# Optimization experiments

Hardware: AMD Instinct MI355X
Metric: run time of the kernel (lower is better)

## Reference

```python
import jax, jax.numpy as jnp
import numpy as np

N, E, NF, EF = 2048, 65536, 128, 64
HID, NH, HD, FF, L = 256, 8, 32, 1024, 4
OUT, MAXN = 1280, 4096


def setup_inputs() -> dict:
    key = jax.random.key(0)
    ks = iter(jax.random.split(key, 64))
    def rn(shape, s=0.02):
        return jax.random.normal(next(ks), shape, jnp.float32) * s
    inp = dict(
        node_features=jax.random.normal(next(ks), (N, NF), jnp.float32),
        edge_features=jax.random.normal(next(ks), (E, EF), jnp.float32),
        edge_index=jax.random.randint(next(ks), (2, E), 0, N),
        W_node=rn((NF, HID)), b_node=jnp.zeros((HID,)),
        W_edge=rn((EF, HID)), b_edge=jnp.zeros((HID,)),
        pos_emb=rn((MAXN, HID), 1.0),
        Wq=rn((L, HID, HID)), bq=jnp.zeros((L, HID)),
        Wk=rn((L, HID, HID)), bk=jnp.zeros((L, HID)),
        Wv=rn((L, HID, HID)), bv=jnp.zeros((L, HID)),
        Wo=rn((L, HID, HID)), bo=jnp.zeros((L, HID)),
        Wep=rn((L, HID, NH)), bep=jnp.zeros((L, NH)),
        Wf1=rn((L, HID, FF)), bf1=jnp.zeros((L, FF)),
        Wf2=rn((L, FF, HID)), bf2=jnp.zeros((L, HID)),
        g1=jnp.ones((L, HID)), be1=jnp.zeros((L, HID)),
        g2=jnp.ones((L, HID)), be2=jnp.zeros((L, HID)),
        g_ln=jnp.ones((HID,)), b_ln=jnp.zeros((HID,)),
        Wp1=rn((HID, HID)), bp1=jnp.zeros((HID,)),
        Wp2=rn((HID, 1)), bp2=jnp.zeros((1,)),
        Wo1=rn((3 * HID, 2 * HID)), bo1=jnp.zeros((2 * HID,)),
        Wo2=rn((2 * HID, OUT)), bo2=jnp.zeros((OUT,)),
    )
    return inp


def _ln(x, g, b, eps=1e-5):
    m = x.mean(-1, keepdims=True)
    v = ((x - m) ** 2).mean(-1, keepdims=True)
    return (x - m) * jax.lax.rsqrt(v + eps) * g + b


def reference(node_features, edge_features, edge_index, W_node, b_node, W_edge,
              b_edge, pos_emb, Wq, bq, Wk, bk, Wv, bv, Wo, bo, Wep, bep,
              Wf1, bf1, Wf2, bf2, g1, be1, g2, be2, g_ln, b_ln,
              Wp1, bp1, Wp2, bp2, Wo1, bo1, Wo2, bo2):
    n = node_features.shape[0]
    src, dst = edge_index[0], edge_index[1]
    scale = float(np.sqrt(HD))
    # node encoding + learned positional embedding (n <= max_nodes path)
    x = node_features @ W_node + b_node + pos_emb[:n]
    edge_attr = edge_features @ W_edge + b_edge  # [E, HID]
    # symmetric adjacency mask with self-loops
    adj = jnp.zeros((n, n), bool).at[src, dst].set(True).at[dst, src].set(True)
    adj = adj.at[jnp.arange(n), jnp.arange(n)].set(True)
    for i in range(L):
        Q = (x @ Wq[i] + bq[i]).reshape(n, NH, HD)
        K = (x @ Wk[i] + bk[i]).reshape(n, NH, HD)
        V = (x @ Wv[i] + bv[i]).reshape(n, NH, HD)
        scores = jnp.einsum('nhd,mhd->nmh', Q, K) / scale  # [n, n, NH]
        ebias = edge_attr @ Wep[i] + bep[i]  # [E, NH]
        scores = scores.at[src, dst].add(ebias)  # accumulating scatter, same as per-edge loop
        scores = jnp.where(adj[:, None, :], scores.transpose(0, 2, 1), -jnp.inf)  # [n, NH, n]
        attn = jax.nn.softmax(scores, axis=-1)
        ctx = jnp.einsum('nhm,mhd->nhd', attn, V).reshape(n, HID)
        a = ctx @ Wo[i] + bo[i]
        x = _ln(x + a, g1[i], be1[i])
        f = jax.nn.gelu(x @ Wf1[i] + bf1[i], approximate=False) @ Wf2[i] + bf2[i]
        x = _ln(x + f, g2[i], be2[i])
    x = _ln(x, g_ln, b_ln)
    # global pooling (batch=None path): mean / max / attention
    mean_p = x.mean(0, keepdims=True)
    max_p = x.max(0, keepdims=True)
    aw = jax.nn.softmax(jnp.tanh(x @ Wp1 + bp1) @ Wp2 + bp2, axis=0)  # [n, 1]
    attn_p = (x * aw).sum(0, keepdims=True)
    g = jnp.concatenate([mean_p, max_p, attn_p], axis=1)  # [1, 3*HID]
    out = jax.nn.relu(g @ Wo1 + bo1) @ Wo2 + bo2  # [1, OUT]
    return out
```

## Files before the change

kernel.cpp:

```cpp
#include <hip/hip_runtime.h>
#include <math.h>

#define NNODE 2048
#define NEDGE 65536
#define HIDN  256
#define NHEAD 8
#define HDIM  32
#define FFD   1024
#define NLAYER 4
#define OUTD  1280
#define NNZ_MAX (2*NEDGE + NNODE)

typedef __attribute__((ext_vector_type(8))) short bf16x8;
typedef __attribute__((ext_vector_type(4))) float f32x4;

__device__ __forceinline__ unsigned short f2b(float f) {
    unsigned u = __float_as_uint(f);
    unsigned r = (u + 0x7fffu + ((u >> 16) & 1u)) >> 16;
    return (unsigned short)r;
}
__device__ __forceinline__ float b2f(unsigned short u) {
    return __uint_as_float((unsigned)u << 16);
}

template<int K, int EPI, int OUT>
__global__ __launch_bounds__(256)
void mgemm(const unsigned short* __restrict__ A, const unsigned short* __restrict__ Bt,
           const float* __restrict__ bias, const float* __restrict__ extra,
           float* __restrict__ Cf, unsigned short* __restrict__ Cb,
           int M, int N, const float* __restrict__ Wp2, float* __restrict__ sred)
{
    __shared__ __align__(16) unsigned short As[64 * 40];
    __shared__ __align__(16) unsigned short Bs[64 * 40];
    int tid = threadIdx.x;
    int bm0 = blockIdx.y * 64, bn0 = blockIdx.x * 64;
    int wave = tid >> 6, lane = tid & 63;
    int wm = (wave >> 1) * 32, wn = (wave & 1) * 32;
    int srow = tid >> 2, skoff = (tid & 3) * 8;
    int lrow = lane & 15, quad = lane >> 4;
    const unsigned short* ap = A  + (size_t)(bm0 + srow) * K + skoff;
    const unsigned short* bp = Bt + (size_t)(bn0 + srow) * K + skoff;
    uint4 av = *(const uint4*)ap;
    uint4 bv = *(const uint4*)bp;
    f32x4 acc[2][2] = {};
    constexpr int NC = K / 32;
    #pragma unroll 8
    for (int c = 0; c < NC; ++c) {
        *(uint4*)(&As[srow*40 + skoff]) = av;
        *(uint4*)(&Bs[srow*40 + skoff]) = bv;
        __syncthreads();
        if (c + 1 < NC) {
            av = *(const uint4*)(ap + (c+1)*32);
            bv = *(const uint4*)(bp + (c+1)*32);
        }
        bf16x8 af[2], bfr[2];
        #pragma unroll
        for (int i = 0; i < 2; i++) af[i]  = *(const bf16x8*)(&As[(wm + i*16 + lrow)*40 + quad*8]);
        #pragma unroll
        for (int j = 0; j < 2; j++) bfr[j] = *(const bf16x8*)(&Bs[(wn + j*16 + lrow)*40 + quad*8]);
        #pragma unroll
        for (int i = 0; i < 2; i++)
            #pragma unroll
            for (int j = 0; j < 2; j++)
                acc[i][j] = __builtin_amdgcn_mfma_f32_16x16x32_bf16(af[i], bfr[j], acc[i][j], 0, 0, 0);
        __syncthreads();
    }
    if (EPI == 4) {
        #pragma unroll
        for (int i = 0; i < 2; i++) {
            #pragma unroll
            for (int r = 0; r < 4; r++) {
                int row = bm0 + wm + i*16 + quad*4 + r;
                float ps = 0.f;
                #pragma unroll
                for (int j = 0; j < 2; j++) {
                    int col = bn0 + wn + j*16 + lrow;
                    float v = tanhf(acc[i][j][r] + bias[col]);
                    ps += v * Wp2[col];
                }
                ps += __shfl_xor(ps, 1);
                ps += __shfl_xor(ps, 2);
                ps += __shfl_xor(ps, 4);
                ps += __shfl_xor(ps, 8);
                if (lrow == 0) atomicAdd(&sred[row], ps);
            }
        }
        return;
    }
    #pragma unroll
    for (int i = 0; i < 2; i++)
        #pragma unroll
        for (int j = 0; j < 2; j++) {
            int col = bn0 + wn + j*16 + lrow;
            float bvv = bias[col];
            #pragma unroll
            for (int r = 0; r < 4; r++) {
                int row = bm0 + wm + i*16 + quad*4 + r;
                float v = acc[i][j][r] + bvv;
                if (EPI == 1) v = 0.5f * v * (1.f + erff(v * 0.70710678118654752f));
                else if (EPI == 2) v = tanhf(v);
                else if (EPI == 3) v += extra[(size_t)row*N + col];
                if (OUT == 0 || OUT == 2) Cf[(size_t)row*N + col] = v;
                if (OUT == 1 || OUT == 2) Cb[(size_t)row*N + col] = f2b(v);
            }
        }
}

__global__ __launch_bounds__(256)
void transpose_all(const float* __restrict__ Wq, const float* __restrict__ Wk,
                   const float* __restrict__ Wv, const float* __restrict__ Wo,
                   const float* __restrict__ Wf1, const float* __restrict__ Wf2,
                   const float* __restrict__ W_node, const float* __restrict__ Wp1,
                   unsigned short* __restrict__ WqkvT, unsigned short* __restrict__ WoT,
                   unsigned short* __restrict__ Wf1T, unsigned short* __restrict__ Wf2T,
                   unsigned short* __restrict__ WnT, unsigned short* __restrict__ Wp1T)
{
    __shared__ unsigned short tile[32][33];
    int bid = blockIdx.x;
    const float* s; unsigned short* d; int K, N, n0, k0;
    if (bid < 1024) {
        int mat = bid >> 6, rem = bid & 63;
        int m4 = mat & 3, l = mat >> 2;
        s = (m4 == 0 ? Wq : m4 == 1 ? Wk : m4 == 2 ? Wv : Wo) + (size_t)l * 65536;
        d = (m4 < 3) ? WqkvT + (size_t)l*196608 + (size_t)m4*65536
                     : WoT + (size_t)l*65536;
        K = 256; N = 256; n0 = (rem & 7) * 32; k0 = (rem >> 3) * 32;
    } else if (bid < 2048) {
        int idx = bid - 1024; int l = idx >> 8, rem = idx & 255;
        s = Wf1 + (size_t)l*262144; d = Wf1T + (size_t)l*262144;
        K = 256; N = 1024; n0 = (rem & 31) * 32; k0 = (rem >> 5) * 32;
    } else if (bid < 3072) {
        int idx = bid - 2048; int l = idx >> 8, rem = idx & 255;
        s = Wf2 + (size_t)l*262144; d = Wf2T + (size_t)l*262144;
        K = 1024; N = 256; n0 = (rem & 7) * 32; k0 = (rem >> 3) * 32;
    } else if (bid < 3104) {
        int rem = bid - 3072;
        s = W_node; d = WnT;
        K = 128; N = 256; n0 = (rem & 7) * 32; k0 = (rem >> 3) * 32;
    } else {
        int rem = bid - 3104;
        s = Wp1; d = Wp1T;
        K = 256; N = 256; n0 = (rem & 7) * 32; k0 = (rem >> 3) * 32;
    }
    int tx = threadIdx.x & 31, ty = threadIdx.x >> 5;
    #pragma unroll
    for (int i = 0; i < 4; i++)
        tile[ty + i*8][tx] = f2b(s[(size_t)(k0 + ty + i*8) * N + n0 + tx]);
    __syncthreads();
    #pragma unroll
    for (int i = 0; i < 4; i++)
        d[(size_t)(n0 + ty + i*8) * K + k0 + tx] = tile[tx][ty + i*8];
}

__global__ void misc_prep(const float* __restrict__ nf, unsigned short* __restrict__ nf_b,
                          const float* __restrict__ bq, const float* __restrict__ bk,
                          const float* __restrict__ bv, float* __restrict__ bqkv)
{
    int t = blockIdx.x * 256 + threadIdx.x;
    if (t < NNODE*128) {
        nf_b[t] = f2b(nf[t]);
    } else {
        int u = t - NNODE*128;
        if (u < NLAYER*768) {
            int l = u / 768, j = u % 768;
            float v = (j < 256) ? bq[l*256 + j] : (j < 512 ? bk[l*256 + j - 256] : bv[l*256 + j - 512]);
            bqkv[u] = v;
        }
    }
}

__global__ void adj_build(const int* __restrict__ src, const int* __restrict__ dst,
                          unsigned* __restrict__ adjbits)
{
    int t = blockIdx.x * blockDim.x + threadIdx.x;
    if (t < NEDGE) {
        int s = src[t], d = dst[t];
        atomicOr(&adjbits[(size_t)s*64 + (d >> 5)], 1u << (d & 31));
        atomicOr(&adjbits[(size_t)d*64 + (s >> 5)], 1u << (s & 31));
    }
    if (t < NNODE)
        atomicOr(&adjbits[(size_t)t*64 + (t >> 5)], 1u << (t & 31));
}

__global__ void row_rank(const unsigned* __restrict__ adjbits,
                         unsigned* __restrict__ rowcum, int* __restrict__ deg)
{
    int i = blockIdx.x * blockDim.x + threadIdx.x;
    if (i >= NNODE) return;
    unsigned c = 0;
    for (int w = 0; w < 64; w++) {
        rowcum[i*64 + w] = c;
        c += __popc(adjbits[i*64 + w]);
    }
    deg[i] = (int)c;
}

__global__ __launch_bounds__(256)
void scan_kernel(const int* __restrict__ deg, int* __restrict__ rowoff)
{
    __shared__ int part[256];
    int tid = threadIdx.x;
    int base = tid * 8;
    int local[8]; int s = 0;
    #pragma unroll
    for (int k = 0; k < 8; k++) { local[k] = s; s += deg[base + k]; }
    part[tid] = s;
    __syncthreads();
    for (int off = 1; off < 256; off <<= 1) {
        int v = (tid >= off) ? part[tid - off] : 0;
        __syncthreads();
        part[tid] += v;
        __syncthreads();
    }
    int pre = (tid == 0) ? 0 : part[tid - 1];
    #pragma unroll
    for (int k = 0; k < 8; k++) rowoff[base + k] = pre + local[k];
    if (tid == 255) rowoff[NNODE] = part[255];
}

__global__ __launch_bounds__(256)
void fill_cols(const unsigned* __restrict__ adjbits, const int* __restrict__ rowoff,
               const unsigned* __restrict__ rowcum, int* __restrict__ cols)
{
    int t = blockIdx.x * 256 + threadIdx.x;
    int i = t >> 6, w = t & 63;
    unsigned bits = adjbits[(size_t)i*64 + w];
    int base = rowoff[i] + (int)rowcum[(size_t)i*64 + w];
    while (bits) {
        int b = __ffs(bits) - 1;
        cols[base++] = w*32 + b;
        bits &= bits - 1;
    }
}

__global__ void wcomb_kernel(const float* __restrict__ W_edge, const float* __restrict__ b_edge,
                             const float* __restrict__ Wep, const float* __restrict__ bep,
                             float* __restrict__ Wcomb, float* __restrict__ bcomb)
{
    int t = blockIdx.x * blockDim.x + threadIdx.x;
    if (t < 64*32) {
        int k = t >> 5, lh = t & 31, l = lh >> 3, h = lh & 7;
        float acc = 0.f;
        for (int c = 0; c < HIDN; c++)
            acc += W_edge[k*HIDN + c] * Wep[l*HIDN*NHEAD + c*NHEAD + h];
        Wcomb[k*32 + lh] = acc;
    } else if (t < 64*32 + 32) {
        int lh = t - 64*32, l = lh >> 3, h = lh & 7;
        float acc = bep[l*NHEAD + h];
        for (int c = 0; c < HIDN; c++)
            acc += b_edge[c] * Wep[l*HIDN*NHEAD + c*NHEAD + h];
        bcomb[lh] = acc;
    }
}

__global__ __launch_bounds__(256)
void edge_bias_scatter(const float* __restrict__ ef, const float* __restrict__ Wcomb,
                       const float* __restrict__ bcomb,
                       const int* __restrict__ src, const int* __restrict__ dst,
                       const unsigned* __restrict__ adjbits,
                       const unsigned* __restrict__ rowcum,
                       const int* __restrict__ rowoff, float* __restrict__ bias_csr)
{
    __shared__ float Wl[64*32];
    __shared__ float bl[32];
    int tid = threadIdx.x;
    for (int k = tid; k < 64*32; k += 256) Wl[k] = Wcomb[k];
    if (tid < 32) bl[tid] = bcomb[tid];
    __syncthreads();
    int t = blockIdx.x * 256 + tid;
    int e = t >> 5, lh = t & 31;
    const float* f = ef + (size_t)e * 64;
    float acc = bl[lh];
    #pragma unroll
    for (int k = 0; k < 64; k++) acc += f[k] * Wl[k*32 + lh];
    int s = src[e], d = dst[e];
    unsigned wbits = adjbits[(size_t)s*64 + (d >> 5)];
    int rank = (int)rowcum[(size_t)s*64 + (d >> 5)] + __popc(wbits & ((1u << (d & 31)) - 1u));
    int slot = rowoff[s] + rank;
    atomicAdd(&bias_csr[(size_t)slot*32 + lh], acc);
}

__global__ __launch_bounds__(256)
void attn_kernel(const unsigned short* __restrict__ QKVb, const int* __restrict__ rowoff,
                 const int* __restrict__ cols, const float* __restrict__ bias_csr,
                 unsigned short* __restrict__ ctxb, int layer)
{
    __shared__ float mS[4][8], lS[4][8];
    __shared__ __align__(16) float accS[4][256];
    int i = blockIdx.x;
    int tid = threadIdx.x;
    int w = tid >> 6, lane = tid & 63;
    int h = lane >> 3;
    int off = lane * 4;
    ushort4 qu = *(const ushort4*)(QKVb + (size_t)i*768 + off);
    float4 qf = { b2f(qu.x), b2f(qu.y), b2f(qu.z), b2f(qu.w) };
    int start = rowoff[i], end = rowoff[i+1];
    int lh0 = layer * 8 + h;
    float m = -INFINITY, l = 0.f;
    float4 acc = {0.f, 0.f, 0.f, 0.f};
    for (int c0 = start + w; c0 < end; c0 += 256) {
        int myslot = c0 + 4*lane;
        int mycol = (myslot < end) ? cols[myslot] : 0;
        int lim = min(end, c0 + 256);
        int it = 0;
        for (int slot = c0; slot < lim; slot += 4, ++it) {
            int j = __shfl(mycol, it);
            ushort4 ku = *(const ushort4*)(QKVb + (size_t)j*768 + 256 + off);
            float s = qf.x*b2f(ku.x) + qf.y*b2f(ku.y) + qf.z*b2f(ku.z) + qf.w*b2f(ku.w);
            s += __shfl_xor(s, 1);
            s += __shfl_xor(s, 2);
            s += __shfl_xor(s, 4);
            s = s * 0.17677669529663687f + bias_csr[(size_t)slot*32 + lh0];
            float mn = fmaxf(m, s);
            float sc = __expf(m - mn);
            float p  = __expf(s - mn);
            ushort4 vu = *(const ushort4*)(QKVb + (size_t)j*768 + 512 + off);
            acc.x = acc.x*sc + p*b2f(vu.x);
            acc.y = acc.y*sc + p*b2f(vu.y);
            acc.z = acc.z*sc + p*b2f(vu.z);
            acc.w = acc.w*sc + p*b2f(vu.w);
            l = l*sc + p;
            m = mn;
        }
    }
    if ((lane & 7) == 0) { mS[w][h] = m; lS[w][h] = l; }
    *(float4*)&accS[w][off] = acc;
    __syncthreads();
    if (w == 0) {
        float m0 = mS[0][h], m1 = mS[1][h], m2 = mS[2][h], m3 = mS[3][h];
        float mx = fmaxf(fmaxf(m0, m1), fmaxf(m2, m3));
        float e0 = (m0 == -INFINITY) ? 0.f : __expf(m0 - mx);
        float e1 = (m1 == -INFINITY) ? 0.f : __expf(m1 - mx);
        float e2 = (m2 == -INFINITY) ? 0.f : __expf(m2 - mx);
        float e3 = (m3 == -INFINITY) ? 0.f : __expf(m3 - mx);
        float ls = lS[0][h]*e0 + lS[1][h]*e1 + lS[2][h]*e2 + lS[3][h]*e3;
        float4 a0 = *(float4*)&accS[0][off];
        float4 a1 = *(float4*)&accS[1][off];
        float4 a2 = *(float4*)&accS[2][off];
        float4 a3 = *(float4*)&accS[3][off];
        float inv = 1.f / ls;
        ushort4 o;
        o.x = f2b((a0.x*e0 + a1.x*e1 + a2.x*e2 + a3.x*e3) * inv);
        o.y = f2b((a0.y*e0 + a1.y*e1 + a2.y*e2 + a3.y*e3) * inv);
        o.z = f2b((a0.z*e0 + a1.z*e1 + a2.z*e2 + a3.z*e3) * inv);
        o.w = f2b((a0.w*e0 + a1.w*e1 + a2.w*e2 + a3.w*e3) * inv);
        *(ushort4*)(ctxb + (size_t)i*HIDN + off) = o;
    }
}

template<bool RES>
__global__ __launch_bounds__(256)
void ln_kernel(float* __restrict__ x, const float* __restrict__ r,
               const float* __restrict__ g, const float* __restrict__ b,
               unsigned short* __restrict__ xb)
{
    __shared__ float lds[4];
    int row = blockIdx.x, c = threadIdx.x;
    float v = x[(size_t)row*HIDN + c];
    if (RES) v += r[(size_t)row*HIDN + c];
    float s = v;
    for (int mm = 1; mm < 64; mm <<= 1) s += __shfl_xor(s, mm);
    if ((c & 63) == 0) lds[c >> 6] = s;
    __syncthreads();
    float mean = (lds[0] + lds[1] + lds[2] + lds[3]) * (1.f / HIDN);
    __syncthreads();
    float dv = v - mean;
    float qq = dv * dv;
    for (int mm = 1; mm < 64; mm <<= 1) qq += __shfl_xor(qq, mm);
    if ((c & 63) == 0) lds[c >> 6] = qq;
    __syncthreads();
    float var = (lds[0] + lds[1] + lds[2] + lds[3]) * (1.f / HIDN);
    float rs = rsqrtf(var + 1e-5f);
    float o = dv * rs * g[c] + b[c];
    x[(size_t)row*HIDN + c] = o;
    xb[(size_t)row*HIDN + c] = f2b(o);
}

__global__ __launch_bounds__(256)
void pool_fused(const float* __restrict__ x, const float* __restrict__ sred,
                float* __restrict__ g)
{
    __shared__ float sl[NNODE];
    __shared__ float red[4];
    __shared__ float l1[4], l2[4], l3[4];
    int c = blockIdx.x, tid = threadIdx.x;
    float mxs = -INFINITY;
    for (int r = tid; r < NNODE; r += 256) {
        float v = sred[r];
        sl[r] = v;
        mxs = fmaxf(mxs, v);
    }
    for (int mm = 1; mm < 64; mm <<= 1) mxs = fmaxf(mxs, __shfl_xor(mxs, mm));
    if ((tid & 63) == 0) red[tid >> 6] = mxs;
    __syncthreads();
    mxs = fmaxf(fmaxf(red[0], red[1]), fmaxf(red[2], red[3]));
    __syncthreads();
    float ss = 0.f;
    for (int r = tid; r < NNODE; r += 256) ss += __expf(sl[r] - mxs);
    for (int mm = 1; mm < 64; mm <<= 1) ss += __shfl_xor(ss, mm);
    if ((tid & 63) == 0) red[tid >> 6] = ss;
    __syncthreads();
    ss = red[0] + red[1] + red[2] + red[3];
    float inv = 1.f / ss;
    float sm = 0.f, mx = -INFINITY, ap = 0.f;
    for (int r = tid; r < NNODE; r += 256) {
        float v = x[(size_t)r*HIDN + c];
        sm += v;
        mx = fmaxf(mx, v);
        ap += v * __expf(sl[r] - mxs) * inv;
    }
    for (int mm = 1; mm < 64; mm <<= 1) {
        sm += __shfl_xor(sm, mm);
        mx = fmaxf(mx, __shfl_xor(mx, mm));
        ap += __shfl_xor(ap, mm);
    }
    if ((tid & 63) == 0) { int w = tid >> 6; l1[w] = sm; l2[w] = mx; l3[w] = ap; }
    __syncthreads();
    if (tid == 0) {
        sm = l1[0] + l1[1] + l1[2] + l1[3];
        mx = fmaxf(fmaxf(l2[0], l2[1]), fmaxf(l2[2], l2[3]));
        ap = l3[0] + l3[1] + l3[2] + l3[3];
        g[c]          = sm * (1.f / NNODE);
        g[HIDN + c]   = mx;
        g[2*HIDN + c] = ap;
    }
}

__global__ __launch_bounds__(512)
void head_fused(const float* __restrict__ g, const float* __restrict__ Wo1,
                const float* __restrict__ bo1, const float* __restrict__ Wo2,
                const float* __restrict__ bo2, float* __restrict__ out)
{
    __shared__ float gs[3*HIDN];
    __shared__ float hs[512];
    int tid = threadIdx.x;
    for (int k = tid; k < 3*HIDN; k += 512) gs[k] = g[k];
    __syncthreads();
    float acc = bo1[tid];
    for (int k = 0; k < 3*HIDN; k++) acc += gs[k] * Wo1[(size_t)k*512 + tid];
    hs[tid] = fmaxf(acc, 0.f);
    __syncthreads();
    for (int j = tid; j < OUTD; j += 512) {
        float a2 = bo2[j];
        for (int k = 0; k < 512; k++) a2 += hs[k] * Wo2[(size_t)k*OUTD + j];
        out[j] = a2;
    }
}

extern "C" void kernel_launch(void* const* d_in, const int* in_sizes, int n_in,
                              void* d_out, int out_size, void* d_ws, size_t ws_size,
                              hipStream_t stream)
{
    const float* node_features = (const float*)d_in[0];
    const float* edge_features = (const float*)d_in[1];
    const int*   edge_index    = (const int*)d_in[2];
    const float* W_node = (const float*)d_in[3];
    const float* b_node = (const float*)d_in[4];
    const float* W_edge = (const float*)d_in[5];
    const float* b_edge = (const float*)d_in[6];
    const float* pos_emb = (const float*)d_in[7];
    const float* Wq = (const float*)d_in[8];
    const float* bq = (const float*)d_in[9];
    const float* Wk = (const float*)d_in[10];
    const float* bk = (const float*)d_in[11];
    const float* Wv = (const float*)d_in[12];
    const float* bv = (const float*)d_in[13];
    const float* Wo = (const float*)d_in[14];
    const float* bo = (const float*)d_in[15];
    const float* Wep = (const float*)d_in[16];
    const float* bep = (const float*)d_in[17];
    const float* Wf1 = (const float*)d_in[18];
    const float* bf1 = (const float*)d_in[19];
    const float* Wf2 = (const float*)d_in[20];
    const float* bf2 = (const float*)d_in[21];
    const float* g1  = (const float*)d_in[22];
    const float* be1 = (const float*)d_in[23];
    const float* g2  = (const float*)d_in[24];
    const float* be2 = (const float*)d_in[25];
    const float* g_ln = (const float*)d_in[26];
    const float* b_ln = (const float*)d_in[27];
    const float* Wp1 = (const float*)d_in[28];
    const float* bp1 = (const float*)d_in[29];
    const float* Wp2 = (const float*)d_in[30];
    const float* bp2 = (const float*)d_in[31];
    const float* Wo1 = (const float*)d_in[32];
    const float* bo1 = (const float*)d_in[33];
    const float* Wo2 = (const float*)d_in[34];
    const float* bo2 = (const float*)d_in[35];
    (void)bp2;
    const int* src = edge_index;
    const int* dst = edge_index + NEDGE;

    char* w = (char*)d_ws;
    auto carve = [&](size_t nbytes) {
        void* p = (void*)w;
        w += (nbytes + 255) & ~(size_t)255;
        return p;
    };
    float* x        = (float*)carve((size_t)NNODE*HIDN*4);
    unsigned short* xb = (unsigned short*)carve((size_t)NNODE*HIDN*2);
    unsigned short* bufQKVb = (unsigned short*)carve((size_t)NNODE*768*2);
    float* bufO     = (float*)carve((size_t)NNODE*HIDN*4);
    unsigned short* bufAb = (unsigned short*)carve((size_t)NNODE*HIDN*2);
    unsigned short* bufFb = (unsigned short*)carve((size_t)NNODE*FFD*2);
    float* Wcomb    = (float*)carve(64*32*4);
    float* bcomb    = (float*)carve(32*4);
    unsigned* adjbits = (unsigned*)carve((size_t)NNODE*64*4);
    float* bias_csr = (float*)carve((size_t)NNZ_MAX*32*4);
    float* sbuf  = (float*)carve(NNODE*4);
    unsigned* rowcum  = (unsigned*)carve((size_t)NNODE*64*4);
    int* deg    = (int*)carve(NNODE*4);
    int* rowoff = (int*)carve((NNODE+1)*4);
    int* colsb  = (int*)carve((size_t)NNZ_MAX*4);
    float* gbuf  = (float*)carve(3*HIDN*4);
    unsigned short* nf_b  = (unsigned short*)carve((size_t)NNODE*128*2);
    unsigned short* WnT   = (unsigned short*)carve((size_t)HIDN*128*2);
    unsigned short* WqkvT = (unsigned short*)carve((size_t)NLAYER*768*HIDN*2);
    float*          bqkv  = (float*)carve((size_t)NLAYER*768*4);
    unsigned short* WoT   = (unsigned short*)carve((size_t)NLAYER*HIDN*HIDN*2);
    unsigned short* Wf1T  = (unsigned short*)carve((size_t)NLAYER*FFD*HIDN*2);
    unsigned short* Wf2T  = (unsigned short*)carve((size_t)NLAYER*HIDN*FFD*2);
    unsigned short* Wp1T  = (unsigned short*)carve((size_t)HIDN*HIDN*2);

    hipMemsetAsync(adjbits, 0,
                   (size_t)NNODE*64*4 + (size_t)NNZ_MAX*32*4 + (size_t)NNODE*4, stream);
    adj_build<<<(NEDGE+255)/256, 256, 0, stream>>>(src, dst, adjbits);
    row_rank<<<NNODE/256, 256, 0, stream>>>(adjbits, rowcum, deg);
    scan_kernel<<<1, 256, 0, stream>>>(deg, rowoff);
    fill_cols<<<(NNODE*64)/256, 256, 0, stream>>>(adjbits, rowoff, rowcum, colsb);
    wcomb_kernel<<<(64*32+32+255)/256, 256, 0, stream>>>(W_edge, b_edge, Wep, bep, Wcomb, bcomb);
    edge_bias_scatter<<<(NEDGE*32)/256, 256, 0, stream>>>(
        edge_features, Wcomb, bcomb, src, dst, adjbits, rowcum, rowoff, bias_csr);

    misc_prep<<<(NNODE*128 + NLAYER*768 + 255)/256, 256, 0, stream>>>(
        node_features, nf_b, bq, bk, bv, bqkv);
    transpose_all<<<3168, 256, 0, stream>>>(Wq, Wk, Wv, Wo, Wf1, Wf2, W_node, Wp1,
                                            WqkvT, WoT, Wf1T, Wf2T, WnT, Wp1T);

    mgemm<128,3,2><<<dim3(HIDN/64, NNODE/64), 256, 0, stream>>>(
        nf_b, WnT, b_node, pos_emb, x, xb, NNODE, HIDN, nullptr, nullptr);

    for (int l = 0; l < NLAYER; l++) {
        mgemm<256,0,1><<<dim3(768/64, NNODE/64), 256, 0, stream>>>(
            xb, WqkvT + (size_t)l*768*HIDN, bqkv + l*768, nullptr, nullptr, bufQKVb, NNODE, 768, nullptr, nullptr);
        attn_kernel<<<NNODE, 256, 0, stream>>>(bufQKVb, rowoff, colsb, bias_csr, bufAb, l);
        mgemm<256,0,0><<<dim3(HIDN/64, NNODE/64), 256, 0, stream>>>(
            bufAb, WoT + (size_t)l*HIDN*HIDN, bo + l*HIDN, nullptr, bufO, nullptr, NNODE, HIDN, nullptr, nullptr);
        ln_kernel<true><<<NNODE, 256, 0, stream>>>(x, bufO, g1 + l*HIDN, be1 + l*HIDN, xb);
        mgemm<256,1,1><<<dim3(FFD/64, NNODE/64), 256, 0, stream>>>(
            xb, Wf1T + (size_t)l*FFD*HIDN, bf1 + l*FFD, nullptr, nullptr, bufFb, NNODE, FFD, nullptr, nullptr);
        mgemm<1024,0,0><<<dim3(HIDN/64, NNODE/64), 256, 0, stream>>>(
            bufFb, Wf2T + (size_t)l*HIDN*FFD, bf2 + l*HIDN, nullptr, bufO, nullptr, NNODE, HIDN, nullptr, nullptr);
        ln_kernel<true><<<NNODE, 256, 0, stream>>>(x, bufO, g2 + l*HIDN, be2 + l*HIDN, xb);
    }

    ln_kernel<false><<<NNODE, 256, 0, stream>>>(x, nullptr, g_ln, b_ln, xb);
    mgemm<256,4,0><<<dim3(HIDN/64, NNODE/64), 256, 0, stream>>>(
        xb, Wp1T, bp1, nullptr, nullptr, nullptr, NNODE, HIDN, Wp2, sbuf);
    pool_fused<<<HIDN, 256, 0, stream>>>(x, sbuf, gbuf);
    head_fused<<<1, 512, 0, stream>>>(gbuf, Wo1, bo1, Wo2, bo2, (float*)d_out);
}
```

Before: 500.7 us.

## Split pooling and output head into coalesced multi-block kernels

Pooling now uses 16 blocks, each handling 128 rows and reading x row-wise with coalesced column accesses, followed by a small finalize kernel. Before, 256 blocks each read one column with a strided pattern. The single-block output head MLP is split into two kernels spread over 8 and 20 blocks, with a K-split across the wavefronts in each block. This trades two extra launches for more parallelism and better memory access in the serial tail.

```diff
diff --git a/kernel.cpp b/kernel.cpp
--- a/kernel.cpp
+++ b/kernel.cpp
@@ -377,74 +377,92 @@
 }
 
 __global__ __launch_bounds__(256)
-void pool_fused(const float* __restrict__ x, const float* __restrict__ sred,
-                float* __restrict__ g)
-{
-    __shared__ float sl[NNODE];
+void pool_part(const float* __restrict__ x, const float* __restrict__ sred,
+               float* __restrict__ partial)
+{
     __shared__ float red[4];
-    __shared__ float l1[4], l2[4], l3[4];
-    int c = blockIdx.x, tid = threadIdx.x;
+    __shared__ float aw[128];
+    int b = blockIdx.x, tid = threadIdx.x;
     float mxs = -INFINITY;
-    for (int r = tid; r < NNODE; r += 256) {
-        float v = sred[r];
-        sl[r] = v;
-        mxs = fmaxf(mxs, v);
-    }
+    for (int r = tid; r < NNODE; r += 256) mxs = fmaxf(mxs, sred[r]);
     for (int mm = 1; mm < 64; mm <<= 1) mxs = fmaxf(mxs, __shfl_xor(mxs, mm));
     if ((tid & 63) == 0) red[tid >> 6] = mxs;
     __syncthreads();
     mxs = fmaxf(fmaxf(red[0], red[1]), fmaxf(red[2], red[3]));
     __syncthreads();
     float ss = 0.f;
-    for (int r = tid; r < NNODE; r += 256) ss += __expf(sl[r] - mxs);
+    for (int r = tid; r < NNODE; r += 256) ss += __expf(sred[r] - mxs);
     for (int mm = 1; mm < 64; mm <<= 1) ss += __shfl_xor(ss, mm);
     if ((tid & 63) == 0) red[tid >> 6] = ss;
     __syncthreads();
     ss = red[0] + red[1] + red[2] + red[3];
     float inv = 1.f / ss;
+    int r0 = b * 128;
+    if (tid < 128) aw[tid] = __expf(sred[r0 + tid] - mxs) * inv;
+    __syncthreads();
     float sm = 0.f, mx = -INFINITY, ap = 0.f;
-    for (int r = tid; r < NNODE; r += 256) {
-        float v = x[(size_t)r*HIDN + c];
+    for (int r = 0; r < 128; r++) {
+        float v = x[(size_t)(r0 + r)*HIDN + tid];
         sm += v;
         mx = fmaxf(mx, v);
-        ap += v * __expf(sl[r] - mxs) * inv;
-    }
-    for (int mm = 1; mm < 64; mm <<= 1) {
-        sm += __shfl_xor(sm, mm);
-        mx = fmaxf(mx, __shfl_xor(mx, mm));
-        ap += __shfl_xor(ap, mm);
-    }
-    if ((tid & 63) == 0) { int w = tid >> 6; l1[w] = sm; l2[w] = mx; l3[w] = ap; }
-    __syncthreads();
-    if (tid == 0) {
-        sm = l1[0] + l1[1] + l1[2] + l1[3];
-        mx = fmaxf(fmaxf(l2[0], l2[1]), fmaxf(l2[2], l2[3]));
-        ap = l3[0] + l3[1] + l3[2] + l3[3];
-        g[c]          = sm * (1.f / NNODE);
-        g[HIDN + c]   = mx;
-        g[2*HIDN + c] = ap;
-    }
-}
-
-__global__ __launch_bounds__(512)
-void head_fused(const float* __restrict__ g, const float* __restrict__ Wo1,
-                const float* __restrict__ bo1, const float* __restrict__ Wo2,
-                const float* __restrict__ bo2, float* __restrict__ out)
-{
-    __shared__ float gs[3*HIDN];
-    __shared__ float hs[512];
+        ap += v * aw[r];
+    }
+    partial[(size_t)b*768 + tid]       = sm;
+    partial[(size_t)b*768 + 256 + tid] = mx;
+    partial[(size_t)b*768 + 512 + tid] = ap;
+}
+
+__global__ __launch_bounds__(256)
+void pool_fin(const float* __restrict__ partial, float* __restrict__ g)
+{
+    int c = threadIdx.x;
+    float sm = 0.f, mx = -INFINITY, ap = 0.f;
+    for (int b = 0; b < 16; b++) {
+        sm += partial[(size_t)b*768 + c];
+        mx = fmaxf(mx, partial[(size_t)b*768 + 256 + c]);
+        ap += partial[(size_t)b*768 + 512 + c];
+    }
+    g[c]          = sm * (1.f / NNODE);
+    g[HIDN + c]   = mx;
+    g[2*HIDN + c] = ap;
+}
+
+__global__ __launch_bounds__(256)
+void head1(const float* __restrict__ g, const float* __restrict__ Wo1,
+           const float* __restrict__ bo1, float* __restrict__ h1)
+{
+    __shared__ float hp[4][64];
     int tid = threadIdx.x;
-    for (int k = tid; k < 3*HIDN; k += 512) gs[k] = g[k];
-    __syncthreads();
-    float acc = bo1[tid];
-    for (int k = 0; k < 3*HIDN; k++) acc += gs[k] * Wo1[(size_t)k*512 + tid];
-    hs[tid] = fmaxf(acc, 0.f);
-    __syncthreads();
-    for (int j = tid; j < OUTD; j += 512) {
-        float a2 = bo2[j];
-        for (int k = 0; k < 512; k++) a2 += hs[k] * Wo2[(size_t)k*OUTD + j];
-        out[j] = a2;
-    }
+    int w = tid >> 6, lane = tid & 63;
+    int j = blockIdx.x * 64 + lane;
+    float acc = 0.f;
+    int k0 = w * 192;
+    for (int k = k0; k < k0 + 192; k++)
+        acc += g[k] * Wo1[(size_t)k*512 + j];
+    hp[w][lane] = acc;
+    __syncthreads();
+    if (w == 0) {
+        float s = hp[0][lane] + hp[1][lane] + hp[2][lane] + hp[3][lane] + bo1[j];
+        h1[j] = fmaxf(s, 0.f);
+    }
+}
+
+__global__ __launch_bounds__(256)
+void head2(const float* __restrict__ h1, const float* __restrict__ Wo2,
+           const float* __restrict__ bo2, float* __restrict__ out)
+{
+    __shared__ float hp[4][64];
+    int tid = threadIdx.x;
+    int w = tid >> 6, lane = tid & 63;
+    int j = blockIdx.x * 64 + lane;
+    float acc = 0.f;
+    int k0 = w * 128;
+    for (int k = k0; k < k0 + 128; k++)
+        acc += h1[k] * Wo2[(size_t)k*OUTD + j];
+    hp[w][lane] = acc;
+    __syncthreads();
+    if (w == 0)
+        out[j] = hp[0][lane] + hp[1][lane] + hp[2][lane] + hp[3][lane] + bo2[j];
 }
 
 extern "C" void kernel_launch(void* const* d_in, const int* in_sizes, int n_in,
@@ -513,6 +531,8 @@
     int* rowoff = (int*)carve((NNODE+1)*4);
     int* colsb  = (int*)carve((size_t)NNZ_MAX*4);
     float* gbuf  = (float*)carve(3*HIDN*4);
+    float* partial = (float*)carve(16*768*4);
+    float* h1buf = (float*)carve(512*4);
     unsigned short* nf_b  = (unsigned short*)carve((size_t)NNODE*128*2);
     unsigned short* WnT   = (unsigned short*)carve((size_t)HIDN*128*2);
     unsigned short* WqkvT = (unsigned short*)carve((size_t)NLAYER*768*HIDN*2);
@@ -557,6 +577,8 @@
     ln_kernel<false><<<NNODE, 256, 0, stream>>>(x, nullptr, g_ln, b_ln, xb);
     mgemm<256,4,0><<<dim3(HIDN/64, NNODE/64), 256, 0, stream>>>(
         xb, Wp1T, bp1, nullptr, nullptr, nullptr, NNODE, HIDN, Wp2, sbuf);
-    pool_fused<<<HIDN, 256, 0, stream>>>(x, sbuf, gbuf);
-    head_fused<<<1, 512, 0, stream>>>(gbuf, Wo1, bo1, Wo2, bo2, (float*)d_out);
-}
+    pool_part<<<16, 256, 0, stream>>>(x, sbuf, partial);
+    pool_fin<<<1, 256, 0, stream>>>(partial, gbuf);
+    head1<<<8, 256, 0, stream>>>(gbuf, Wo1, bo1, h1buf);
+    head2<<<OUTD/64, 256, 0, stream>>>(h1buf, Wo2, bo2, (float*)d_out);
+}
```

After: 462.4 us. -7.7%, faster.
